# Kernel tuning notes

Hardware: AMD Instinct MI355X
Metric: run time of the kernel (lower is better)

The kernel has to match this reference:

```python
import jax, jax.numpy as jnp
import numpy as np

B, S, D = 2, 2048, 1024
H = 16
HD = D // H
MLP = 4096
EPS = 1e-5


def _layernorm(x, g, b):
    mu = jnp.mean(x, axis=-1, keepdims=True)
    var = jnp.mean(jnp.square(x - mu), axis=-1, keepdims=True)
    return (x - mu) * jax.lax.rsqrt(var + EPS) * g + b


def setup_inputs() -> dict:
    key = jax.random.key(0)
    ks = jax.random.split(key, 16)
    sd = 0.02
    return {
        "x": jax.random.normal(ks[0], (B, S, D), jnp.float32),
        "dis_attn_mask": jax.random.normal(ks[1], (B, S, S), jnp.float32) * 0.1,
        "cls_attn_mask": jax.random.normal(ks[2], (B, S, S), jnp.float32) * 0.1,
        "wq": jax.random.normal(ks[3], (D, D), jnp.float32) * sd,
        "bq": jnp.zeros((D,), jnp.float32),
        "wk": jax.random.normal(ks[4], (D, D), jnp.float32) * sd,
        "bk": jnp.zeros((D,), jnp.float32),
        "wv": jax.random.normal(ks[5], (D, D), jnp.float32) * sd,
        "bv": jnp.zeros((D,), jnp.float32),
        "ln1_g": jnp.ones((D,), jnp.float32),
        "ln1_b": jnp.zeros((D,), jnp.float32),
        "ln2_g": jnp.ones((D,), jnp.float32),
        "ln2_b": jnp.zeros((D,), jnp.float32),
        "w1": jax.random.normal(ks[6], (D, MLP), jnp.float32) * sd,
        "b1": jnp.zeros((MLP,), jnp.float32),
        "w2": jax.random.normal(ks[7], (MLP, D), jnp.float32) * sd,
        "b2": jnp.zeros((D,), jnp.float32),
    }


def reference(x, dis_attn_mask, cls_attn_mask, wq, bq, wk, bk, wv, bv,
              ln1_g, ln1_b, ln2_g, ln2_b, w1, b1, w2, b2):
    res = x
    h = _layernorm(x, ln1_g, ln1_b)
    q = h @ wq + bq
    k = h @ wk + bk
    v = h @ wv + bv
    # NOTE: original torch code uses .view(B, H, S, HD) on a contiguous
    # [B, S, D] tensor (no transpose); row-major reshape reproduces this.
    q = q.reshape(B, H, S, HD)
    k = k.reshape(B, H, S, HD)
    v = v.reshape(B, H, S, HD)
    w = jnp.einsum('bhsd,bhtd->bhst', q, k) * (HD ** -0.5)
    w = w + dis_attn_mask[:, None] + cls_attn_mask[:, None]
    w = jax.nn.softmax(w, axis=-1)
    h_attn = jnp.einsum('bhst,bhtd->bhsd', w, v).reshape(B, S, D)
    h = h_attn + res
    h = _layernorm(h, ln2_g, ln2_b)
    res2 = h
    h = jax.nn.gelu(h @ w1 + b1, approximate=False) @ w2 + b2
    return h + res2
```

## Files before the change

### kernel.cpp

```cpp
#include <hip/hip_runtime.h>
#include <hip/hip_bf16.h>
#include <math.h>

#define BB 2
#define SS 2048
#define DD 1024
#define HH 16
#define MLPD 4096

typedef __attribute__((ext_vector_type(8))) short bf16x8;
typedef __attribute__((ext_vector_type(4))) float f32x4;
typedef __attribute__((ext_vector_type(4))) unsigned short us4;

static __device__ __forceinline__ float fast_exp2(float x) {
#if __has_builtin(__builtin_amdgcn_exp2f)
  return __builtin_amdgcn_exp2f(x);
#else
  return exp2f(x);
#endif
}
static __device__ __forceinline__ float fast_rcp(float x) {
#if __has_builtin(__builtin_amdgcn_rcpf)
  return __builtin_amdgcn_rcpf(x);
#else
  return 1.0f / x;
#endif
}

static __device__ __forceinline__ unsigned short f2bf(float f) {
  union { float f; unsigned int u; } v; v.f = f;
  unsigned int r = v.u + 0x7fffu + ((v.u >> 16) & 1u);
  return (unsigned short)(r >> 16);
}
static __device__ __forceinline__ float bf2f(unsigned short b) {
  return __uint_as_float(((unsigned int)b) << 16);
}

static __device__ __forceinline__ float gelu_f(float x) {
  float u = x * x;
  float z = x * fmaf(u, 0.0713548162f, 1.59576912f);
  float e = fast_exp2(z * -1.44269504f);
  return x * fast_rcp(1.0f + e);
}

static __device__ __forceinline__ int swz(int row) {
  return (row & 3) ^ ((row >> 2) & 3);
}

static __device__ __forceinline__ void async16(const unsigned short* g, unsigned short* l) {
  __builtin_amdgcn_global_load_lds(
      (const __attribute__((address_space(1))) unsigned int*)g,
      (__attribute__((address_space(3))) unsigned int*)l, 16, 0, 0);
}

__global__ __launch_bounds__(256) void transpose_to_bf16(
    const float* __restrict__ src, unsigned short* __restrict__ dst,
    int K, int N) {
  __shared__ float tile[32][33];
  int t = threadIdx.x;
  int c = t & 31, rl = t >> 5;
  int bx = blockIdx.x, by = blockIdx.y;
#pragma unroll
  for (int i = 0; i < 4; ++i) {
    int row = rl * 4 + i;
    tile[row][c] = src[(size_t)(by * 32 + row) * N + bx * 32 + c];
  }
  __syncthreads();
#pragma unroll
  for (int i = 0; i < 4; ++i) {
    int n = rl * 4 + i;
    dst[(size_t)(bx * 32 + n) * K + by * 32 + c] = f2bf(tile[c][n]);
  }
}

__global__ __launch_bounds__(256) void transpose_qkv(
    const float* __restrict__ wq, const float* __restrict__ wk,
    const float* __restrict__ wv, unsigned short* __restrict__ dst) {
  __shared__ float tile[32][33];
  const float* src = blockIdx.z == 0 ? wq : blockIdx.z == 1 ? wk : wv;
  unsigned short* d = dst + (size_t)blockIdx.z * 1024 * 1024;
  int t = threadIdx.x;
  int c = t & 31, rl = t >> 5;
  int bx = blockIdx.x, by = blockIdx.y;
#pragma unroll
  for (int i = 0; i < 4; ++i) {
    int row = rl * 4 + i;
    tile[row][c] = src[(size_t)(by * 32 + row) * DD + bx * 32 + c];
  }
  __syncthreads();
#pragma unroll
  for (int i = 0; i < 4; ++i) {
    int n = rl * 4 + i;
    d[(size_t)(bx * 32 + n) * DD + by * 32 + c] = f2bf(tile[c][n]);
  }
}

__global__ __launch_bounds__(256) void concat_bias(
    const float* __restrict__ bq, const float* __restrict__ bk,
    const float* __restrict__ bv, float* __restrict__ dst) {
  int i = blockIdx.x * 256 + threadIdx.x;
  if (i < 1024) dst[i] = bq[i];
  else if (i < 2048) dst[i] = bk[i - 1024];
  else if (i < 3072) dst[i] = bv[i - 2048];
}

__global__ __launch_bounds__(256) void mask_prep(
    const float* __restrict__ dis, const float* __restrict__ cls,
    unsigned short* __restrict__ cm) {
  size_t i = ((size_t)blockIdx.x * 256 + threadIdx.x) * 4;
  float4 d = *(const float4*)(dis + i);
  float4 c = *(const float4*)(cls + i);
  us4 o;
  o[0] = f2bf((d.x + c.x) * 1.44269504f);
  o[1] = f2bf((d.y + c.y) * 1.44269504f);
  o[2] = f2bf((d.z + c.z) * 1.44269504f);
  o[3] = f2bf((d.w + c.w) * 1.44269504f);
  *(us4*)(cm + i) = o;
}

template <bool BF_IN, bool ADD>
__global__ __launch_bounds__(256) void ln_bf16(
    const void* __restrict__ in, const float* __restrict__ add,
    const float* __restrict__ g, const float* __restrict__ beta,
    unsigned short* __restrict__ out) {
  int row = blockIdx.x;
  int t = threadIdx.x;
  float x[4];
  if (BF_IN) {
    us4 b4 = *(const us4*)((const unsigned short*)in + (size_t)row * DD + t * 4);
#pragma unroll
    for (int i = 0; i < 4; ++i) x[i] = bf2f(b4[i]);
  } else {
    float4 f4 = *(const float4*)((const float*)in + (size_t)row * DD + t * 4);
    x[0] = f4.x; x[1] = f4.y; x[2] = f4.z; x[3] = f4.w;
  }
  if (ADD) {
    float4 a4 = *(const float4*)(add + (size_t)row * DD + t * 4);
    x[0] += a4.x; x[1] += a4.y; x[2] += a4.z; x[3] += a4.w;
  }
  float s1 = x[0] + x[1] + x[2] + x[3];
  float s2 = x[0] * x[0] + x[1] * x[1] + x[2] * x[2] + x[3] * x[3];
#pragma unroll
  for (int off = 32; off > 0; off >>= 1) {
    s1 += __shfl_down(s1, off);
    s2 += __shfl_down(s2, off);
  }
  __shared__ float sa[4], sb[4];
  int wid = t >> 6;
  if ((t & 63) == 0) { sa[wid] = s1; sb[wid] = s2; }
  __syncthreads();
  s1 = sa[0] + sa[1] + sa[2] + sa[3];
  s2 = sb[0] + sb[1] + sb[2] + sb[3];
  float mean = s1 * (1.0f / 1024.0f);
  float var = s2 * (1.0f / 1024.0f) - mean * mean;
  float rstd = rsqrtf(var + 1e-5f);
  float4 gv = *(const float4*)(g + t * 4);
  float4 bv = *(const float4*)(beta + t * 4);
  us4 o;
  o[0] = f2bf((x[0] - mean) * rstd * gv.x + bv.x);
  o[1] = f2bf((x[1] - mean) * rstd * gv.y + bv.y);
  o[2] = f2bf((x[2] - mean) * rstd * gv.z + bv.z);
  o[3] = f2bf((x[3] - mean) * rstd * gv.w + bv.w);
  *(us4*)(out + (size_t)row * DD + t * 4) = o;
}

template <int BN, bool GELU, bool ADDSRC, bool OUT_BF16, bool SPLIT3>
__global__ __launch_bounds__(256) void gemm_bf16(
    const unsigned short* __restrict__ A, const unsigned short* __restrict__ BT,
    const float* __restrict__ bias, const unsigned short* __restrict__ addsrc,
    void* C0, void* C1, void* C2, int M, int N, int K) {
  constexpr int BJ = BN / 32;
  constexpr int BCH = BN / 64;
  __shared__ __align__(16) unsigned short As[128][32];
  __shared__ __align__(16) unsigned short Bs[BN][32];
  int tid = threadIdx.x;
  int wave = tid >> 6, lane = tid & 63;
  int g = lane >> 4, c16 = lane & 15;
  int m0 = blockIdx.y * 128, n0 = blockIdx.x * BN;
  int wm = (wave >> 1) * 64, wn = (wave & 1) * (BN / 2);
  int lrow = lane >> 2, lq = lane & 3;
  int dq = (lq ^ swz(lrow)) * 8;
  const unsigned short* aS = A + (size_t)(m0 + wave * 32 + lrow) * K + lq * 8;
  unsigned short* aD0 = &As[wave * 32 + lrow][dq];
  unsigned short* aD1 = &As[wave * 32 + 16 + lrow][dq];
  const unsigned short* bS = BT + (size_t)(n0 + wave * (BCH * 16) + lrow) * K + lq * 8;
  unsigned short* bD0 = &Bs[wave * (BCH * 16) + lrow][dq];
  unsigned short* bD1 = &Bs[(wave * (BCH * 16) + 16 + lrow) % BN][dq];
  int vA = (g ^ swz(c16)) * 8;
  const int KI = K / 32;
  const size_t rK = 16 * (size_t)K;

  bf16x8 a0a = *(const bf16x8*)(aS);
  bf16x8 a1a = *(const bf16x8*)(aS + rK);
  bf16x8 b0a = *(const bf16x8*)(bS);
  bf16x8 b1a;
  if constexpr (BCH == 2) b1a = *(const bf16x8*)(bS + rK);
  bf16x8 a0b = *(const bf16x8*)(aS + 32);
  bf16x8 a1b = *(const bf16x8*)(aS + rK + 32);
  bf16x8 b0b = *(const bf16x8*)(bS + 32);
  bf16x8 b1b;
  if constexpr (BCH == 2) b1b = *(const bf16x8*)(bS + rK + 32);

  f32x4 acc[4][BJ] = {};
  for (int kt = 0; kt < KI; kt += 2) {
    __syncthreads();
    *(bf16x8*)aD0 = a0a;
    *(bf16x8*)aD1 = a1a;
    *(bf16x8*)bD0 = b0a;
    if constexpr (BCH == 2) *(bf16x8*)bD1 = b1a;
    __syncthreads();
    if (kt + 2 < KI) {
      int ko = (kt + 2) * 32;
      a0a = *(const bf16x8*)(aS + ko);
      a1a = *(const bf16x8*)(aS + rK + ko);
      b0a = *(const bf16x8*)(bS + ko);
      if constexpr (BCH == 2) b1a = *(const bf16x8*)(bS + rK + ko);
    }
    {
      bf16x8 a[4], b[BJ];
#pragma unroll
      for (int i = 0; i < 4; ++i) a[i] = *(const bf16x8*)&As[wm + i * 16 + c16][vA];
#pragma unroll
      for (int j = 0; j < BJ; ++j) b[j] = *(const bf16x8*)&Bs[wn + j * 16 + c16][vA];
#pragma unroll
      for (int i = 0; i < 4; ++i)
#pragma unroll
        for (int j = 0; j < BJ; ++j)
          acc[i][j] = __builtin_amdgcn_mfma_f32_16x16x32_bf16(a[i], b[j], acc[i][j], 0, 0, 0);
    }
    __syncthreads();
    *(bf16x8*)aD0 = a0b;
    *(bf16x8*)aD1 = a1b;
    *(bf16x8*)bD0 = b0b;
    if constexpr (BCH == 2) *(bf16x8*)bD1 = b1b;
    __syncthreads();
    if (kt + 3 < KI) {
      int ko = (kt + 3) * 32;
      a0b = *(const bf16x8*)(aS + ko);
      a1b = *(const bf16x8*)(aS + rK + ko);
      b0b = *(const bf16x8*)(bS + ko);
      if constexpr (BCH == 2) b1b = *(const bf16x8*)(bS + rK + ko);
    }
    {
      bf16x8 a[4], b[BJ];
#pragma unroll
      for (int i = 0; i < 4; ++i) a[i] = *(const bf16x8*)&As[wm + i * 16 + c16][vA];
#pragma unroll
      for (int j = 0; j < BJ; ++j) b[j] = *(const bf16x8*)&Bs[wn + j * 16 + c16][vA];
#pragma unroll
      for (int i = 0; i < 4; ++i)
#pragma unroll
        for (int j = 0; j < BJ; ++j)
          acc[i][j] = __builtin_amdgcn_mfma_f32_16x16x32_bf16(a[i], b[j], acc[i][j], 0, 0, 0);
    }
  }
  unsigned short* dstb = nullptr;
  int lc0 = 0;
  if (SPLIT3) {
    int which = n0 >> 10;
    dstb = (unsigned short*)(which == 0 ? C0 : which == 1 ? C1 : C2);
    lc0 = n0 & 1023;
  }
#pragma unroll
  for (int j = 0; j < BJ; ++j) {
    int coff = wn + j * 16 + c16;
    float bj = bias[n0 + coff];
#pragma unroll
    for (int i = 0; i < 4; ++i) {
#pragma unroll
      for (int r = 0; r < 4; ++r) {
        int row = m0 + wm + i * 16 + g * 4 + r;
        float cval = acc[i][j][r] + bj;
        if (GELU) cval = gelu_f(cval);
        if (ADDSRC) cval += bf2f(addsrc[(size_t)row * N + n0 + coff]);
        if (SPLIT3) {
          dstb[(size_t)row * 1024 + lc0 + coff] = f2bf(cval);
        } else if (OUT_BF16) {
          ((unsigned short*)C0)[(size_t)row * N + n0 + coff] = f2bf(cval);
        } else {
          ((float*)C0)[(size_t)row * N + n0 + coff] = cval;
        }
      }
    }
  }
}

#define VMW(n) asm volatile("s_waitcnt vmcnt(" #n ")" ::: "memory")
#define BARX() do { asm volatile("" ::: "memory"); \
                    __builtin_amdgcn_s_barrier(); \
                    asm volatile("" ::: "memory"); } while (0)

template <bool GELU, bool SPLIT3>
__global__ __launch_bounds__(512, 2) void gemm256(
    const unsigned short* __restrict__ A, const unsigned short* __restrict__ BT,
    const float* __restrict__ bias, void* C0, void* C1, void* C2,
    int N, int K) {
  __shared__ __align__(16) char lds[2][2][2][16384];
  int tid = threadIdx.x;
  int lane = tid & 63, w = tid >> 6;
  int g = lane >> 4, c16 = lane & 15;
  int wm16 = (w >> 2) << 4;
  int wn16 = (w & 3) << 4;
  int m0 = blockIdx.y << 8, n0 = blockIdx.x << 8;

  int st0 = tid >> 6, ci0 = tid & 63;
  int cp0 = ci0 ^ (((ci0 >> 5) & 1) << 1);
  int sr0 = ((st0 >> 1) << 4) + (cp0 >> 2);
  int sk0 = ((st0 & 1) << 5) + ((cp0 & 3) << 3);
  size_t soff = (size_t)sr0 * K + sk0;

  auto stage = [&](int op, int h, int tt, int d) {
    const unsigned short* base = (op == 0 ? A : BT);
    int row0 = (op == 0 ? m0 : n0) + (h << 7);
    const unsigned short* src = base + (size_t)row0 * K + (tt << 6) + soff;
    unsigned short* dst = (unsigned short*)&lds[op][d][h][tid * 16];
    async16(src, dst);
    async16(src + ((size_t)K << 6), dst + 4096);
  };

  auto foff = [&](int r, int ke) -> int {
    int stt = ((r >> 4) << 1) + (ke >> 5);
    int loc = ((r & 15) << 6) + ((ke & 31) << 1);
    return (stt << 10) + (loc ^ (((r >> 3) & 1) << 5));
  };
  int offA[4][2], offB[2][2];
#pragma unroll
  for (int ii = 0; ii < 4; ++ii)
#pragma unroll
    for (int ks = 0; ks < 2; ++ks)
      offA[ii][ks] = foff(ii * 32 + wm16 + c16, ks * 32 + g * 8);
#pragma unroll
  for (int jj = 0; jj < 2; ++jj)
#pragma unroll
    for (int ks = 0; ks < 2; ++ks)
      offB[jj][ks] = foff(jj * 64 + wn16 + c16, ks * 32 + g * 8);

  f32x4 acc[8][4] = {};

#define MFMA_Q(IH, JH, AF, BF) do {                                           \
    __builtin_amdgcn_s_setprio(1);                                            \
    _Pragma("unroll") for (int ii = 0; ii < 4; ++ii)                          \
      _Pragma("unroll") for (int jj = 0; jj < 2; ++jj) {                      \
        acc[(IH)*4+ii][(JH)*2+jj] = __builtin_amdgcn_mfma_f32_16x16x32_bf16(  \
            AF[ii][0], BF[jj][0], acc[(IH)*4+ii][(JH)*2+jj], 0, 0, 0);        \
        acc[(IH)*4+ii][(JH)*2+jj] = __builtin_amdgcn_mfma_f32_16x16x32_bf16(  \
            AF[ii][1], BF[jj][1], acc[(IH)*4+ii][(JH)*2+jj], 0, 0, 0);        \
      }                                                                       \
    __builtin_amdgcn_s_setprio(0);                                            \
  } while (0)

  stage(0, 0, 0, 0);
  stage(1, 0, 0, 0);
  stage(0, 1, 0, 0);
  stage(1, 1, 0, 0);
  VMW(4);
  BARX();

  const int KT = K >> 6;
  for (int kt = 0; kt < KT; ++kt) {
    int d = kt & 1, dn = d ^ 1;
    int t1 = kt + 1 < KT ? kt + 1 : KT - 1;
    const char* pd = &lds[0][d][0][0];
    bf16x8 A0f[4][2], A1f[4][2], Bf[2][2];

#pragma unroll
    for (int ii = 0; ii < 4; ++ii)
#pragma unroll
      for (int ks = 0; ks < 2; ++ks)
        A0f[ii][ks] = *(const bf16x8*)(pd + offA[ii][ks]);
#pragma unroll
    for (int jj = 0; jj < 2; ++jj)
#pragma unroll
      for (int ks = 0; ks < 2; ++ks)
        Bf[jj][ks] = *(const bf16x8*)(pd + 65536 + offB[jj][ks]);
    stage(0, 0, t1, dn);
    VMW(4);
    BARX();
    MFMA_Q(0, 0, A0f, Bf);
    BARX();

#pragma unroll
    for (int ii = 0; ii < 4; ++ii)
#pragma unroll
      for (int ks = 0; ks < 2; ++ks)
        A1f[ii][ks] = *(const bf16x8*)(pd + 16384 + offA[ii][ks]);
    stage(1, 0, t1, dn);
    VMW(4);
    BARX();
    MFMA_Q(1, 0, A1f, Bf);
    BARX();

#pragma unroll
    for (int jj = 0; jj < 2; ++jj)
#pragma unroll
      for (int ks = 0; ks < 2; ++ks)
        Bf[jj][ks] = *(const bf16x8*)(pd + 81920 + offB[jj][ks]);
    stage(0, 1, t1, dn);
    VMW(4);
    BARX();
    MFMA_Q(1, 1, A1f, Bf);
    BARX();

    stage(1, 1, t1, dn);
    VMW(4);
    BARX();
    MFMA_Q(0, 1, A0f, Bf);
    BARX();
  }
#undef MFMA_Q
  VMW(0);

  unsigned short* dstb = nullptr;
  int lc0 = 0;
  if (SPLIT3) {
    int which = n0 >> 10;
    dstb = (unsigned short*)(which == 0 ? C0 : which == 1 ? C1 : C2);
    lc0 = n0 & 1023;
  }
#pragma unroll
  for (int i = 0; i < 8; ++i) {
#pragma unroll
    for (int j = 0; j < 4; ++j) {
      int row_b = m0 + ((i >> 2) << 7) + ((i & 3) << 5) + wm16 + (g << 2);
      int colp = ((j >> 1) << 7) + ((j & 1) << 6) + wn16 + c16;
      float bj = bias[n0 + colp];
#pragma unroll
      for (int r = 0; r < 4; ++r) {
        float cv = acc[i][j][r] + bj;
        if (GELU) cv = gelu_f(cv);
        int row = row_b + r;
        if (SPLIT3) {
          dstb[(size_t)row * 1024 + lc0 + colp] = f2bf(cv);
        } else {
          ((unsigned short*)C0)[(size_t)row * N + n0 + colp] = f2bf(cv);
        }
      }
    }
  }
}

__global__ __launch_bounds__(512) void attn_mfma(
    const unsigned short* __restrict__ q, const unsigned short* __restrict__ k,
    const unsigned short* __restrict__ v, const unsigned short* __restrict__ cm,
    unsigned short* __restrict__ outO) {
  __shared__ __align__(16) unsigned short Ks[2][64][32];
  __shared__ __align__(16) unsigned short Vt[64][72];
  __shared__ __align__(16) unsigned short Ps[128][72];
  int tid = threadIdx.x;
  int wave = tid >> 6, lane = tid & 63;
  int g = lane >> 4, c16 = lane & 15;
  int qt = blockIdx.x, h = blockIdx.y, b = blockIdx.z;
  int s0 = qt * 128;
  int wr = wave * 16;
  size_t headoff = (size_t)b * SS * DD + (size_t)h * SS * 64;
  const unsigned short* qb = q + headoff;
  const unsigned short* kb = k + headoff;
  const unsigned short* vb = v + headoff;
  const unsigned short* cmb = cm + (size_t)b * SS * SS;

  int kkey = tid >> 3, kseg = tid & 7;
  unsigned short* kdst = &Ks[kseg >> 2][kkey][((kseg & 3) ^ swz(kkey)) * 8];
  const unsigned short* ksrc = kb + (size_t)kkey * 64 + kseg * 8;
  const unsigned short* vsrc = vb + (size_t)lane * 64 + wave * 8;
  int vK = (g ^ swz(c16)) * 8;

  bf16x8 qf0, qf1;
  {
    size_t qrow = (size_t)(s0 + wr + c16) * 64;
    qf0 = *(const bf16x8*)(qb + qrow + g * 8);
    qf1 = *(const bf16x8*)(qb + qrow + 32 + g * 8);
  }
  bf16x8 ones;
#pragma unroll
  for (int j = 0; j < 8; ++j) ones[j] = (short)0x3F80;
  f32x4 o[4] = {};
  f32x4 ol = {};
  const float scale2 = 0.18033688f;

  bf16x8 kreg = *(const bf16x8*)(ksrc);
  bf16x8 vreg = *(const bf16x8*)(vsrc);
  unsigned short cmc[4][4];
#pragma unroll
  for (int t = 0; t < 4; ++t)
#pragma unroll
    for (int r = 0; r < 4; ++r)
      cmc[t][r] = cmb[(size_t)(s0 + wr + g * 4 + r) * SS + t * 16 + c16];

  for (int kt = 0; kt < 32; ++kt) {
    __syncthreads();
    *(bf16x8*)kdst = kreg;
#pragma unroll
    for (int j = 0; j < 8; ++j) Vt[wave * 8 + j][lane] = (unsigned short)vreg[j];
    __syncthreads();

    int ktn = kt + 1 < 32 ? kt + 1 : 31;
    bf16x8 kregN = *(const bf16x8*)(ksrc + (size_t)ktn * 4096);
    bf16x8 vregN = *(const bf16x8*)(vsrc + (size_t)ktn * 4096);
    unsigned short cmN[4][4];
#pragma unroll
    for (int t = 0; t < 4; ++t)
#pragma unroll
      for (int r = 0; r < 4; ++r)
        cmN[t][r] = cmb[(size_t)(s0 + wr + g * 4 + r) * SS + ktn * 64 + t * 16 + c16];

    f32x4 s[4] = {};
#pragma unroll
    for (int t = 0; t < 4; ++t) {
      bf16x8 b0 = *(const bf16x8*)&Ks[0][t * 16 + c16][vK];
      bf16x8 b1 = *(const bf16x8*)&Ks[1][t * 16 + c16][vK];
      s[t] = __builtin_amdgcn_mfma_f32_16x16x32_bf16(qf0, b0, s[t], 0, 0, 0);
      s[t] = __builtin_amdgcn_mfma_f32_16x16x32_bf16(qf1, b1, s[t], 0, 0, 0);
    }
#pragma unroll
    for (int t = 0; t < 4; ++t)
#pragma unroll
      for (int r = 0; r < 4; ++r) {
        float p = fast_exp2(fmaf(s[t][r], scale2, bf2f(cmc[t][r])));
        Ps[wr + g * 4 + r][t * 16 + c16] = (unsigned short)(__float_as_uint(p) >> 16);
      }
#pragma unroll
    for (int ks = 0; ks < 2; ++ks) {
      bf16x8 pa = *(const bf16x8*)&Ps[wr + c16][ks * 32 + g * 8];
#pragma unroll
      for (int t2 = 0; t2 < 4; ++t2) {
        bf16x8 vb8 = *(const bf16x8*)&Vt[t2 * 16 + c16][ks * 32 + g * 8];
        o[t2] = __builtin_amdgcn_mfma_f32_16x16x32_bf16(pa, vb8, o[t2], 0, 0, 0);
      }
      ol = __builtin_amdgcn_mfma_f32_16x16x32_bf16(pa, ones, ol, 0, 0, 0);
    }
    kreg = kregN;
    vreg = vregN;
#pragma unroll
    for (int t = 0; t < 4; ++t)
#pragma unroll
      for (int r = 0; r < 4; ++r) cmc[t][r] = cmN[t][r];
  }
  float inv[4];
#pragma unroll
  for (int r = 0; r < 4; ++r) inv[r] = fast_rcp(ol[r]);
#pragma unroll
  for (int t2 = 0; t2 < 4; ++t2)
#pragma unroll
    for (int r = 0; r < 4; ++r) {
      int srow = s0 + wr + g * 4 + r;
      outO[headoff + (size_t)srow * 64 + t2 * 16 + c16] = f2bf(o[t2][r] * inv[r]);
    }
}

extern "C" void kernel_launch(void* const* d_in, const int* in_sizes, int n_in,
                              void* d_out, int out_size, void* d_ws, size_t ws_size,
                              hipStream_t stream) {
  const float* x    = (const float*)d_in[0];
  const float* dis  = (const float*)d_in[1];
  const float* cls  = (const float*)d_in[2];
  const float* wq   = (const float*)d_in[3];
  const float* bq   = (const float*)d_in[4];
  const float* wk   = (const float*)d_in[5];
  const float* bk   = (const float*)d_in[6];
  const float* wv   = (const float*)d_in[7];
  const float* bv   = (const float*)d_in[8];
  const float* ln1g = (const float*)d_in[9];
  const float* ln1b = (const float*)d_in[10];
  const float* ln2g = (const float*)d_in[11];
  const float* ln2b = (const float*)d_in[12];
  const float* w1   = (const float*)d_in[13];
  const float* b1   = (const float*)d_in[14];
  const float* w2   = (const float*)d_in[15];
  const float* b2   = (const float*)d_in[16];
  float* out = (float*)d_out;
  char* ws = (char*)d_ws;

  unsigned short* qkvwT = (unsigned short*)(ws + 0);
  unsigned short* w1T   = (unsigned short*)(ws + 6291456);
  unsigned short* w2T   = (unsigned short*)(ws + 14680064);
  float*          qkvb  = (float*)(ws + 23068672);
  unsigned short* r1    = (unsigned short*)(ws + 23134208);
  unsigned short* qbuf  = (unsigned short*)(ws + 31522816);
  unsigned short* kbuf  = (unsigned short*)(ws + 39911424);
  unsigned short* vbuf  = (unsigned short*)(ws + 48300032);
  unsigned short* h2    = (unsigned short*)(ws + 56688640);
  unsigned short* cmb   = (unsigned short*)(ws + 65077248);
  unsigned short* mm    = (unsigned short*)(ws + 23134208);
  unsigned short* h1 = r1;
  unsigned short* attnO = r1;

  const int rows = BB * SS;

  transpose_qkv<<<dim3(DD / 32, DD / 32, 3), 256, 0, stream>>>(wq, wk, wv, qkvwT);
  transpose_to_bf16<<<dim3(MLPD / 32, DD / 32), 256, 0, stream>>>(w1, w1T, DD, MLPD);
  transpose_to_bf16<<<dim3(DD / 32, MLPD / 32), 256, 0, stream>>>(w2, w2T, MLPD, DD);
  concat_bias<<<12, 256, 0, stream>>>(bq, bk, bv, qkvb);
  mask_prep<<<8192, 256, 0, stream>>>(dis, cls, cmb);

  ln_bf16<false, false><<<rows, 256, 0, stream>>>(x, nullptr, ln1g, ln1b, h1);

  gemm256<false, true><<<dim3(3072 / 256, rows / 256), 512, 0, stream>>>(
      h1, qkvwT, qkvb, qbuf, kbuf, vbuf, 3072, DD);

  attn_mfma<<<dim3(SS / 128, HH, BB), 512, 0, stream>>>(qbuf, kbuf, vbuf, cmb, attnO);

  ln_bf16<true, true><<<rows, 256, 0, stream>>>(attnO, x, ln2g, ln2b, h2);

  gemm256<true, false><<<dim3(MLPD / 256, rows / 256), 512, 0, stream>>>(
      h2, w1T, b1, mm, nullptr, nullptr, MLPD, DD);

  gemm_bf16<64, false, true, false, false><<<dim3(DD / 64, rows / 128), 256, 0, stream>>>(
      mm, w2T, b2, h2, out, nullptr, nullptr, rows, DD, MLPD);
}
```

Before: 402.0 us.

## Pre-pack attention mask into MFMA fragment layout and seed accumulators with it

The mask prep kernel now writes the combined dis+cls mask in a per-block, per-wave, per-lane packed layout. The attention kernel can then fetch each thread's 16 mask values per key tile with two 16-byte loads instead of sixteen scattered 2-byte loads. The mask is pre-scaled so it can initialise the QK^T accumulators directly, which removes the fma from the softmax exponent. In exchange, the new prep kernel reads the fp32 masks with scalar strided loads over fewer blocks, which may make the prep step slower.

```diff
diff --git a/kernel.cpp b/kernel.cpp
--- a/kernel.cpp
+++ b/kernel.cpp
@@ -104,18 +104,34 @@
   else if (i < 3072) dst[i] = bv[i - 2048];
 }
 
-__global__ __launch_bounds__(256) void mask_prep(
+__global__ __launch_bounds__(256) void mask_prep2(
     const float* __restrict__ dis, const float* __restrict__ cls,
-    unsigned short* __restrict__ cm) {
-  size_t i = ((size_t)blockIdx.x * 256 + threadIdx.x) * 4;
-  float4 d = *(const float4*)(dis + i);
-  float4 c = *(const float4*)(cls + i);
-  us4 o;
-  o[0] = f2bf((d.x + c.x) * 1.44269504f);
-  o[1] = f2bf((d.y + c.y) * 1.44269504f);
-  o[2] = f2bf((d.z + c.z) * 1.44269504f);
-  o[3] = f2bf((d.w + c.w) * 1.44269504f);
-  *(us4*)(cm + i) = o;
+    unsigned short* __restrict__ cmP) {
+  int qt = blockIdx.x, wave = blockIdx.y, b = blockIdx.z;
+  int tid = threadIdx.x;
+  int ktg = tid >> 6, lane = tid & 63;
+  int g = lane >> 4, c16 = lane & 15;
+  const float* db = dis + (size_t)b * SS * SS;
+  const float* cb = cls + (size_t)b * SS * SS;
+  unsigned short* ob =
+      cmP + ((((size_t)b * 16 + qt) * 8 + wave) * 32) * 64 * 16;
+  int row0 = qt * 128 + wave * 16 + g * 4;
+#pragma unroll
+  for (int i = 0; i < 8; ++i) {
+    int kt = ktg * 8 + i;
+    int col0 = kt * 64 + c16;
+    short v[16];
+#pragma unroll
+    for (int t = 0; t < 4; ++t)
+#pragma unroll
+      for (int r = 0; r < 4; ++r) {
+        size_t idx = (size_t)(row0 + r) * SS + col0 + t * 16;
+        v[t * 4 + r] = (short)f2bf((db[idx] + cb[idx]) * 8.0f);
+      }
+    unsigned short* o = ob + ((size_t)kt * 64 + lane) * 16;
+    *(bf16x8*)(o) = *(bf16x8*)&v[0];
+    *(bf16x8*)(o + 8) = *(bf16x8*)&v[8];
+  }
 }
 
 template <bool BF_IN, bool ADD>
@@ -441,7 +457,7 @@
 
 __global__ __launch_bounds__(512) void attn_mfma(
     const unsigned short* __restrict__ q, const unsigned short* __restrict__ k,
-    const unsigned short* __restrict__ v, const unsigned short* __restrict__ cm,
+    const unsigned short* __restrict__ v, const unsigned short* __restrict__ cmP,
     unsigned short* __restrict__ outO) {
   __shared__ __align__(16) unsigned short Ks[2][64][32];
   __shared__ __align__(16) unsigned short Vt[64][72];
@@ -456,7 +472,8 @@
   const unsigned short* qb = q + headoff;
   const unsigned short* kb = k + headoff;
   const unsigned short* vb = v + headoff;
-  const unsigned short* cmb = cm + (size_t)b * SS * SS;
+  const unsigned short* csrc =
+      cmP + ((((size_t)b * 16 + qt) * 8 + wave) * 32 * 64 + lane) * 16;
 
   int kkey = tid >> 3, kseg = tid & 7;
   unsigned short* kdst = &Ks[kseg >> 2][kkey][((kseg & 3) ^ swz(kkey)) * 8];
@@ -479,12 +496,8 @@
 
   bf16x8 kreg = *(const bf16x8*)(ksrc);
   bf16x8 vreg = *(const bf16x8*)(vsrc);
-  unsigned short cmc[4][4];
-#pragma unroll
-  for (int t = 0; t < 4; ++t)
-#pragma unroll
-    for (int r = 0; r < 4; ++r)
-      cmc[t][r] = cmb[(size_t)(s0 + wr + g * 4 + r) * SS + t * 16 + c16];
+  bf16x8 cmA = *(const bf16x8*)(csrc);
+  bf16x8 cmB = *(const bf16x8*)(csrc + 8);
 
   for (int kt = 0; kt < 32; ++kt) {
     __syncthreads();
@@ -496,14 +509,17 @@
     int ktn = kt + 1 < 32 ? kt + 1 : 31;
     bf16x8 kregN = *(const bf16x8*)(ksrc + (size_t)ktn * 4096);
     bf16x8 vregN = *(const bf16x8*)(vsrc + (size_t)ktn * 4096);
-    unsigned short cmN[4][4];
-#pragma unroll
-    for (int t = 0; t < 4; ++t)
-#pragma unroll
-      for (int r = 0; r < 4; ++r)
-        cmN[t][r] = cmb[(size_t)(s0 + wr + g * 4 + r) * SS + ktn * 64 + t * 16 + c16];
-
-    f32x4 s[4] = {};
+    bf16x8 cmAN = *(const bf16x8*)(csrc + (size_t)ktn * 1024);
+    bf16x8 cmBN = *(const bf16x8*)(csrc + (size_t)ktn * 1024 + 8);
+
+    f32x4 s[4];
+#pragma unroll
+    for (int r = 0; r < 4; ++r) {
+      s[0][r] = bf2f((unsigned short)cmA[r]);
+      s[1][r] = bf2f((unsigned short)cmA[4 + r]);
+      s[2][r] = bf2f((unsigned short)cmB[r]);
+      s[3][r] = bf2f((unsigned short)cmB[4 + r]);
+    }
 #pragma unroll
     for (int t = 0; t < 4; ++t) {
       bf16x8 b0 = *(const bf16x8*)&Ks[0][t * 16 + c16][vK];
@@ -515,7 +531,7 @@
     for (int t = 0; t < 4; ++t)
 #pragma unroll
       for (int r = 0; r < 4; ++r) {
-        float p = fast_exp2(fmaf(s[t][r], scale2, bf2f(cmc[t][r])));
+        float p = fast_exp2(s[t][r] * scale2);
         Ps[wr + g * 4 + r][t * 16 + c16] = (unsigned short)(__float_as_uint(p) >> 16);
       }
 #pragma unroll
@@ -530,10 +546,8 @@
     }
     kreg = kregN;
     vreg = vregN;
-#pragma unroll
-    for (int t = 0; t < 4; ++t)
-#pragma unroll
-      for (int r = 0; r < 4; ++r) cmc[t][r] = cmN[t][r];
+    cmA = cmAN;
+    cmB = cmBN;
   }
   float inv[4];
 #pragma unroll
@@ -579,7 +593,7 @@
   unsigned short* kbuf  = (unsigned short*)(ws + 39911424);
   unsigned short* vbuf  = (unsigned short*)(ws + 48300032);
   unsigned short* h2    = (unsigned short*)(ws + 56688640);
-  unsigned short* cmb   = (unsigned short*)(ws + 65077248);
+  unsigned short* cmP   = (unsigned short*)(ws + 65077248);
   unsigned short* mm    = (unsigned short*)(ws + 23134208);
   unsigned short* h1 = r1;
   unsigned short* attnO = r1;
@@ -590,14 +604,14 @@
   transpose_to_bf16<<<dim3(MLPD / 32, DD / 32), 256, 0, stream>>>(w1, w1T, DD, MLPD);
   transpose_to_bf16<<<dim3(DD / 32, MLPD / 32), 256, 0, stream>>>(w2, w2T, MLPD, DD);
   concat_bias<<<12, 256, 0, stream>>>(bq, bk, bv, qkvb);
-  mask_prep<<<8192, 256, 0, stream>>>(dis, cls, cmb);
+  mask_prep2<<<dim3(SS / 128, 8, BB), 256, 0, stream>>>(dis, cls, cmP);
 
   ln_bf16<false, false><<<rows, 256, 0, stream>>>(x, nullptr, ln1g, ln1b, h1);
 
   gemm256<false, true><<<dim3(3072 / 256, rows / 256), 512, 0, stream>>>(
       h1, qkvwT, qkvb, qbuf, kbuf, vbuf, 3072, DD);
 
-  attn_mfma<<<dim3(SS / 128, HH, BB), 512, 0, stream>>>(qbuf, kbuf, vbuf, cmb, attnO);
+  attn_mfma<<<dim3(SS / 128, HH, BB), 512, 0, stream>>>(qbuf, kbuf, vbuf, cmP, attnO);
 
   ln_bf16<true, true><<<rows, 256, 0, stream>>>(attnO, x, ln2g, ln2b, h2);
 
```

Result: slower. 412.3 us (+2.6%).
